# Optimization experiments

Measured on AMD Instinct MI355X. Metric: run time of the kernel, lower is better.

## Reference

```python
import jax, jax.numpy as jnp
import numpy as np

B, LQ, LK, DQ, DK, DV, H = 4, 256, 512, 256, 256, 256, 128


def setup_inputs() -> dict:
    key = jax.random.key(0)
    kq, kk, kv, kwq, kwk, kwv, kl = jax.random.split(key, 7)
    queries = jax.random.normal(kq, (B, LQ, DQ), dtype=jnp.float32)
    keys = jax.random.normal(kk, (B, LK, DK), dtype=jnp.float32)
    values = jax.random.normal(kv, (B, LK, DV), dtype=jnp.float32)
    # Lazy linear params (no bias): W_q: DQ->H, W_k: DK->H, w_v: H->1
    Wq = jax.random.normal(kwq, (DQ, H), dtype=jnp.float32) / np.sqrt(DQ)
    Wk = jax.random.normal(kwk, (DK, H), dtype=jnp.float32) / np.sqrt(DK)
    wv = jax.random.normal(kwv, (H,), dtype=jnp.float32) / np.sqrt(H)
    valid_lens = jax.random.randint(kl, (B,), 1, LK + 1)
    return {"queries": queries, "keys": keys, "values": values,
            "Wq": Wq, "Wk": Wk, "wv": wv, "valid_lens": valid_lens}


def reference(queries, keys, values, Wq, Wk, wv, valid_lens):
    q = jnp.einsum('bqd,dh->bqh', queries, Wq)          # [B,LQ,H]
    k = jnp.einsum('bkd,dh->bkh', keys, Wk)             # [B,LK,H]
    # broadcast-add -> tanh -> reduce over H (the big [B,LQ,LK,H] intermediate)
    features = jnp.tanh(q[:, :, None, :] + k[:, None, :, :])
    scores = jnp.einsum('bqkh,h->bqk', features, wv)    # [B,LQ,LK]
    # masked_softmax with per-batch valid lengths (d2l semantics: masked -> -1e6)
    mask = jnp.arange(scores.shape[-1])[None, None, :] < valid_lens[:, None, None]
    scores = jnp.where(mask, scores, jnp.float32(-1e6))
    attn = jax.nn.softmax(scores, axis=-1)              # [B,LQ,LK]
    return jnp.einsum('bqk,bkv->bqv', attn, values)     # [B,LQ,DV]
```

## Files before the change

### kernel.cpp

```cpp
#include <hip/hip_runtime.h>

#define B_   4
#define LQ_  256
#define LK_  512
#define DQK_ 256
#define DV_  256
#define H_   128

#define TANH_C 2.8853900817779268f
#define L2E    1.4426950408889634f
#define NQBLK (B_ * LQ_ / 4)
#define NKBLK (B_ * LK_ / 4)

__global__ __launch_bounds__(128) void proj_kernel(const float* __restrict__ Q,
                                                   const float* __restrict__ K,
                                                   const float* __restrict__ Wq,
                                                   const float* __restrict__ Wk,
                                                   float* __restrict__ eq,
                                                   float* __restrict__ ekT) {
    const int blk = blockIdx.x;
    const bool isq = blk < NQBLK;
    const float* in = isq ? Q  : K;
    const float* W  = isq ? Wq : Wk;
    const int r0 = (isq ? blk : blk - NQBLK) * 4;
    const int t  = threadIdx.x;

    float acc0 = 0.f, acc1 = 0.f, acc2 = 0.f, acc3 = 0.f;
    const float4* in4 = reinterpret_cast<const float4*>(in + (size_t)r0 * DQK_);
    for (int d4 = 0; d4 < DQK_ / 4; ++d4) {
        float4 r0v = in4[0 * (DQK_ / 4) + d4];
        float4 r1v = in4[1 * (DQK_ / 4) + d4];
        float4 r2v = in4[2 * (DQK_ / 4) + d4];
        float4 r3v = in4[3 * (DQK_ / 4) + d4];
#pragma unroll
        for (int e = 0; e < 4; ++e) {
            float w = W[(size_t)(4 * d4 + e) * H_ + t];
            acc0 = fmaf(reinterpret_cast<const float*>(&r0v)[e], w, acc0);
            acc1 = fmaf(reinterpret_cast<const float*>(&r1v)[e], w, acc1);
            acc2 = fmaf(reinterpret_cast<const float*>(&r2v)[e], w, acc2);
            acc3 = fmaf(reinterpret_cast<const float*>(&r3v)[e], w, acc3);
        }
    }
    float e0 = __builtin_amdgcn_exp2f(acc0 * TANH_C);
    float e1 = __builtin_amdgcn_exp2f(acc1 * TANH_C);
    float e2 = __builtin_amdgcn_exp2f(acc2 * TANH_C);
    float e3 = __builtin_amdgcn_exp2f(acc3 * TANH_C);
    if (isq) {
        eq[(size_t)(r0 + 0) * H_ + t] = e0;
        eq[(size_t)(r0 + 1) * H_ + t] = e1;
        eq[(size_t)(r0 + 2) * H_ + t] = e2;
        eq[(size_t)(r0 + 3) * H_ + t] = e3;
    } else {
        const int b  = r0 >> 9;
        const int k0 = r0 & (LK_ - 1);
        float* o = ekT + ((size_t)(b * H_ + t)) * LK_ + k0;
        *reinterpret_cast<float4*>(o) = make_float4(e0, e1, e2, e3);
    }
}

__global__ __launch_bounds__(1024) void attn_kernel(
    const float* __restrict__ eq,
    const float* __restrict__ ekT,
    const float* __restrict__ wv,
    const float* __restrict__ values,
    const int*   __restrict__ valid_lens,
    float* __restrict__ out) {
    __shared__ float eq_l[4][H_];
    __shared__ float wm2[H_];
    __shared__ float sc[LK_][4];
    __shared__ float part[4][4][DV_];
    __shared__ float red[20];
    __shared__ float inv_s[4];

    const int blk = blockIdx.x;
    const int b   = blk >> 6;
    const int qt  = blk & 63;
    const int t   = threadIdx.x;

    if (t < 512) {
        eq_l[t >> 7][t & 127] = eq[(size_t)(b * LQ_ + qt * 4 + (t >> 7)) * H_ + (t & 127)];
    } else if (t < 640) {
        wm2[t - 512] = -2.f * wv[t - 512];
    }
    __syncthreads();

    const int valid = valid_lens[b];

    {
        const int k    = t & 511;
        const int pair = __builtin_amdgcn_readfirstlane(t >> 9);
        float2 s2 = make_float2(-1e6f, -1e6f);
        if (k < valid) {
            const float* ekp = ekT + (size_t)b * H_ * LK_ + k;
            const float4* w4  = reinterpret_cast<const float4*>(wm2);
            const float4* qa4 = reinterpret_cast<const float4*>(eq_l[2 * pair]);
            const float4* qb4 = reinterpret_cast<const float4*>(eq_l[2 * pair + 1]);
            float p0 = 0.f, p1 = 0.f;
#pragma unroll 4
            for (int h4 = 0; h4 < H_ / 4; ++h4) {
                float4 w  = w4[h4];
                float4 qa = qa4[h4];
                float4 qb = qb4[h4];
#pragma unroll
                for (int e = 0; e < 4; ++e) {
                    float ek = ekp[(size_t)(4 * h4 + e) * LK_];
                    float fa = fmaf(reinterpret_cast<const float*>(&qa)[e], ek, 1.f);
                    float fb = fmaf(reinterpret_cast<const float*>(&qb)[e], ek, 1.f);
                    float ww = reinterpret_cast<const float*>(&w)[e];
                    p0 = fmaf(ww, __builtin_amdgcn_rcpf(fa), p0);
                    p1 = fmaf(ww, __builtin_amdgcn_rcpf(fb), p1);
                }
            }
            s2 = make_float2(p0, p1);
        }
        *reinterpret_cast<float2*>(&sc[k][2 * pair]) = s2;
    }
    __syncthreads();

    const int qi = t >> 8;
    const int kl = t & 255;
    float s0 = sc[kl][qi], s1 = sc[kl + 256][qi];
    {
        float m = fmaxf(s0, s1);
#pragma unroll
        for (int off = 32; off; off >>= 1) m = fmaxf(m, __shfl_down(m, off, 64));
        if ((t & 63) == 0) red[t >> 6] = m;
    }
    __syncthreads();
    if (t < 4) {
        red[16 + t] = fmaxf(fmaxf(red[4 * t], red[4 * t + 1]),
                            fmaxf(red[4 * t + 2], red[4 * t + 3]));
    }
    __syncthreads();
    {
        const float m = red[16 + qi];
        float e0 = __builtin_amdgcn_exp2f((s0 - m) * L2E);
        float e1 = __builtin_amdgcn_exp2f((s1 - m) * L2E);
        sc[kl][qi]       = e0;
        sc[kl + 256][qi] = e1;
        float ss = e0 + e1;
#pragma unroll
        for (int off = 32; off; off >>= 1) ss += __shfl_down(ss, off, 64);
        if ((t & 63) == 0) red[t >> 6] = ss;
    }
    __syncthreads();
    if (t < 4) {
        inv_s[t] = 1.f / (red[4 * t] + red[4 * t + 1] + red[4 * t + 2] + red[4 * t + 3]);
    }
    __syncthreads();

    {
        const int kh = __builtin_amdgcn_readfirstlane(t >> 8);
        const int v  = t & 255;
        const int kstart = kh * 128;
        const int kend   = min(kstart + 128, valid);
        const float* vb = values + (size_t)b * LK_ * DV_ + v;
        float a0 = 0.f, a1 = 0.f, a2 = 0.f, a3 = 0.f;
#pragma unroll 4
        for (int k = kstart; k < kend; ++k) {
            float4 f  = *reinterpret_cast<const float4*>(&sc[k][0]);
            float val = vb[(size_t)k * DV_];
            a0 = fmaf(f.x, val, a0);
            a1 = fmaf(f.y, val, a1);
            a2 = fmaf(f.z, val, a2);
            a3 = fmaf(f.w, val, a3);
        }
        part[kh][0][v] = a0;
        part[kh][1][v] = a1;
        part[kh][2][v] = a2;
        part[kh][3][v] = a3;
    }
    __syncthreads();
    {
        const int v = t & 255;
        float r = (part[0][qi][v] + part[1][qi][v]) + (part[2][qi][v] + part[3][qi][v]);
        out[(size_t)(b * LQ_ + qt * 4 + qi) * DV_ + v] = r * inv_s[qi];
    }
}

extern "C" void kernel_launch(void* const* d_in, const int* in_sizes, int n_in,
                              void* d_out, int out_size, void* d_ws, size_t ws_size,
                              hipStream_t stream) {
    const float* queries    = (const float*)d_in[0];
    const float* keys       = (const float*)d_in[1];
    const float* values     = (const float*)d_in[2];
    const float* Wq         = (const float*)d_in[3];
    const float* Wk         = (const float*)d_in[4];
    const float* wv         = (const float*)d_in[5];
    const int*   valid_lens = (const int*)d_in[6];
    float* out = (float*)d_out;

    float* eq  = (float*)d_ws;
    float* ekT = eq + (size_t)B_ * LQ_ * H_;

    proj_kernel<<<NQBLK + NKBLK, 128, 0, stream>>>(queries, keys, Wq, Wk, eq, ekT);
    attn_kernel<<<B_ * LQ_ / 4, 1024, 0, stream>>>(eq, ekT, wv, values, valid_lens, out);
}
```

Before: 30.44 us.

## Retile projection to 8 rows via LDS and attention to 2 queries per block

The projection kernel now stages 8 input rows in shared memory and computes 8 outputs per thread, halving the block count and reusing each weight load across more rows. The attention kernel is retiled to 512-thread blocks handling 2 queries each, with every thread scoring 2 adjacent keys via float2 loads. The block index is swizzled so adjacent blocks interleave batches. The eq/wv staging in LDS is dropped in favour of direct uniform loads. The aim is better occupancy and more blocks, at the cost of each block re-reading ekT and values for only 2 queries, which doubles global traffic for those tensors.

Measured after the change: 41.54 us. 36.4% more time.

```diff
diff --git a/kernel.cpp b/kernel.cpp
--- a/kernel.cpp
+++ b/kernel.cpp
@@ -9,8 +9,8 @@
 
 #define TANH_C 2.8853900817779268f
 #define L2E    1.4426950408889634f
-#define NQBLK (B_ * LQ_ / 4)
-#define NKBLK (B_ * LK_ / 4)
+#define NQBLK (B_ * LQ_ / 8)
+#define NKBLK (B_ * LK_ / 8)
 
 __global__ __launch_bounds__(128) void proj_kernel(const float* __restrict__ Q,
                                                    const float* __restrict__ K,
@@ -18,108 +18,94 @@
                                                    const float* __restrict__ Wk,
                                                    float* __restrict__ eq,
                                                    float* __restrict__ ekT) {
+    __shared__ float rows[8 * DQK_];
     const int blk = blockIdx.x;
     const bool isq = blk < NQBLK;
     const float* in = isq ? Q  : K;
     const float* W  = isq ? Wq : Wk;
-    const int r0 = (isq ? blk : blk - NQBLK) * 4;
+    const int r0 = (isq ? blk : blk - NQBLK) * 8;
     const int t  = threadIdx.x;
 
-    float acc0 = 0.f, acc1 = 0.f, acc2 = 0.f, acc3 = 0.f;
     const float4* in4 = reinterpret_cast<const float4*>(in + (size_t)r0 * DQK_);
+    float4* r4 = reinterpret_cast<float4*>(rows);
+#pragma unroll
+    for (int i = 0; i < 4; ++i) r4[t + 128 * i] = in4[t + 128 * i];
+    __syncthreads();
+
+    float acc[8];
+#pragma unroll
+    for (int j = 0; j < 8; ++j) acc[j] = 0.f;
+
+#pragma unroll 2
     for (int d4 = 0; d4 < DQK_ / 4; ++d4) {
-        float4 r0v = in4[0 * (DQK_ / 4) + d4];
-        float4 r1v = in4[1 * (DQK_ / 4) + d4];
-        float4 r2v = in4[2 * (DQK_ / 4) + d4];
-        float4 r3v = in4[3 * (DQK_ / 4) + d4];
+        float w0 = W[(size_t)(4 * d4 + 0) * H_ + t];
+        float w1 = W[(size_t)(4 * d4 + 1) * H_ + t];
+        float w2 = W[(size_t)(4 * d4 + 2) * H_ + t];
+        float w3 = W[(size_t)(4 * d4 + 3) * H_ + t];
 #pragma unroll
-        for (int e = 0; e < 4; ++e) {
-            float w = W[(size_t)(4 * d4 + e) * H_ + t];
-            acc0 = fmaf(reinterpret_cast<const float*>(&r0v)[e], w, acc0);
-            acc1 = fmaf(reinterpret_cast<const float*>(&r1v)[e], w, acc1);
-            acc2 = fmaf(reinterpret_cast<const float*>(&r2v)[e], w, acc2);
-            acc3 = fmaf(reinterpret_cast<const float*>(&r3v)[e], w, acc3);
+        for (int j = 0; j < 8; ++j) {
+            float4 r = *reinterpret_cast<const float4*>(&rows[j * DQK_ + 4 * d4]);
+            acc[j] = fmaf(r.x, w0, fmaf(r.y, w1, fmaf(r.z, w2, fmaf(r.w, w3, acc[j]))));
         }
     }
-    float e0 = __builtin_amdgcn_exp2f(acc0 * TANH_C);
-    float e1 = __builtin_amdgcn_exp2f(acc1 * TANH_C);
-    float e2 = __builtin_amdgcn_exp2f(acc2 * TANH_C);
-    float e3 = __builtin_amdgcn_exp2f(acc3 * TANH_C);
+    float e[8];
+#pragma unroll
+    for (int j = 0; j < 8; ++j) e[j] = __builtin_amdgcn_exp2f(acc[j] * TANH_C);
+
     if (isq) {
-        eq[(size_t)(r0 + 0) * H_ + t] = e0;
-        eq[(size_t)(r0 + 1) * H_ + t] = e1;
-        eq[(size_t)(r0 + 2) * H_ + t] = e2;
-        eq[(size_t)(r0 + 3) * H_ + t] = e3;
+#pragma unroll
+        for (int j = 0; j < 8; ++j)
+            eq[(size_t)(r0 + j) * H_ + t] = e[j];
     } else {
         const int b  = r0 >> 9;
         const int k0 = r0 & (LK_ - 1);
         float* o = ekT + ((size_t)(b * H_ + t)) * LK_ + k0;
-        *reinterpret_cast<float4*>(o) = make_float4(e0, e1, e2, e3);
+        *reinterpret_cast<float4*>(o)     = make_float4(e[0], e[1], e[2], e[3]);
+        *reinterpret_cast<float4*>(o + 4) = make_float4(e[4], e[5], e[6], e[7]);
     }
 }
 
-__global__ __launch_bounds__(1024) void attn_kernel(
+__global__ __launch_bounds__(512, 4) void attn_kernel(
     const float* __restrict__ eq,
     const float* __restrict__ ekT,
     const float* __restrict__ wv,
     const float* __restrict__ values,
     const int*   __restrict__ valid_lens,
     float* __restrict__ out) {
-    __shared__ float eq_l[4][H_];
-    __shared__ float wm2[H_];
-    __shared__ float sc[LK_][4];
-    __shared__ float part[4][4][DV_];
-    __shared__ float red[20];
-    __shared__ float inv_s[4];
+    __shared__ float sc[LK_][2];
+    __shared__ float part[2][2][DV_];
+    __shared__ float red[8];
+    __shared__ float redm[2];
+    __shared__ float inv_s[2];
 
     const int blk = blockIdx.x;
-    const int b   = blk >> 6;
-    const int qt  = blk & 63;
+    const int b   = (blk & 1) | (((blk >> 8) & 1) << 1);
+    const int qt  = (blk >> 1) & 127;
     const int t   = threadIdx.x;
-
-    if (t < 512) {
-        eq_l[t >> 7][t & 127] = eq[(size_t)(b * LQ_ + qt * 4 + (t >> 7)) * H_ + (t & 127)];
-    } else if (t < 640) {
-        wm2[t - 512] = -2.f * wv[t - 512];
-    }
-    __syncthreads();
-
     const int valid = valid_lens[b];
 
+    const int qi = __builtin_amdgcn_readfirstlane(t >> 8);
+    const int kq = t & 255;
+
+    float s0 = -1e6f, s1 = -1e6f;
     {
-        const int k    = t & 511;
-        const int pair = __builtin_amdgcn_readfirstlane(t >> 9);
-        float2 s2 = make_float2(-1e6f, -1e6f);
-        if (k < valid) {
-            const float* ekp = ekT + (size_t)b * H_ * LK_ + k;
-            const float4* w4  = reinterpret_cast<const float4*>(wm2);
-            const float4* qa4 = reinterpret_cast<const float4*>(eq_l[2 * pair]);
-            const float4* qb4 = reinterpret_cast<const float4*>(eq_l[2 * pair + 1]);
+        const float* eqr = eq + (size_t)(b * LQ_ + qt * 2 + qi) * H_;
+        const float* ekp = ekT + (size_t)b * H_ * LK_ + 2 * kq;
+        if (2 * kq < valid) {
             float p0 = 0.f, p1 = 0.f;
-#pragma unroll 4
-            for (int h4 = 0; h4 < H_ / 4; ++h4) {
-                float4 w  = w4[h4];
-                float4 qa = qa4[h4];
-                float4 qb = qb4[h4];
-#pragma unroll
-                for (int e = 0; e < 4; ++e) {
-                    float ek = ekp[(size_t)(4 * h4 + e) * LK_];
-                    float fa = fmaf(reinterpret_cast<const float*>(&qa)[e], ek, 1.f);
-                    float fb = fmaf(reinterpret_cast<const float*>(&qb)[e], ek, 1.f);
-                    float ww = reinterpret_cast<const float*>(&w)[e];
-                    p0 = fmaf(ww, __builtin_amdgcn_rcpf(fa), p0);
-                    p1 = fmaf(ww, __builtin_amdgcn_rcpf(fb), p1);
-                }
+#pragma unroll 8
+            for (int h = 0; h < H_; ++h) {
+                float2 ek = *reinterpret_cast<const float2*>(ekp + (size_t)h * LK_);
+                float q = eqr[h];
+                float w = wv[h];
+                p0 = fmaf(w, __builtin_amdgcn_rcpf(fmaf(q, ek.x, 1.f)), p0);
+                p1 = fmaf(w, __builtin_amdgcn_rcpf(fmaf(q, ek.y, 1.f)), p1);
             }
-            s2 = make_float2(p0, p1);
+            s0 = -2.f * p0;
+            s1 = (2 * kq + 1 < valid) ? -2.f * p1 : -1e6f;
         }
-        *reinterpret_cast<float2*>(&sc[k][2 * pair]) = s2;
     }
-    __syncthreads();
 
-    const int qi = t >> 8;
-    const int kl = t & 255;
-    float s0 = sc[kl][qi], s1 = sc[kl + 256][qi];
     {
         float m = fmaxf(s0, s1);
 #pragma unroll
@@ -127,54 +113,48 @@
         if ((t & 63) == 0) red[t >> 6] = m;
     }
     __syncthreads();
-    if (t < 4) {
-        red[16 + t] = fmaxf(fmaxf(red[4 * t], red[4 * t + 1]),
-                            fmaxf(red[4 * t + 2], red[4 * t + 3]));
+    if (t < 2) {
+        redm[t] = fmaxf(fmaxf(red[4 * t], red[4 * t + 1]),
+                        fmaxf(red[4 * t + 2], red[4 * t + 3]));
     }
     __syncthreads();
     {
-        const float m = red[16 + qi];
+        const float m = redm[qi];
         float e0 = __builtin_amdgcn_exp2f((s0 - m) * L2E);
         float e1 = __builtin_amdgcn_exp2f((s1 - m) * L2E);
-        sc[kl][qi]       = e0;
-        sc[kl + 256][qi] = e1;
+        sc[2 * kq][qi]     = e0;
+        sc[2 * kq + 1][qi] = e1;
         float ss = e0 + e1;
 #pragma unroll
         for (int off = 32; off; off >>= 1) ss += __shfl_down(ss, off, 64);
         if ((t & 63) == 0) red[t >> 6] = ss;
     }
     __syncthreads();
-    if (t < 4) {
+    if (t < 2) {
         inv_s[t] = 1.f / (red[4 * t] + red[4 * t + 1] + red[4 * t + 2] + red[4 * t + 3]);
     }
     __syncthreads();
 
     {
-        const int kh = __builtin_amdgcn_readfirstlane(t >> 8);
-        const int v  = t & 255;
-        const int kstart = kh * 128;
-        const int kend   = min(kstart + 128, valid);
+        const int v    = t & 255;
+        const int half = t >> 8;
         const float* vb = values + (size_t)b * LK_ * DV_ + v;
-        float a0 = 0.f, a1 = 0.f, a2 = 0.f, a3 = 0.f;
-#pragma unroll 4
-        for (int k = kstart; k < kend; ++k) {
-            float4 f  = *reinterpret_cast<const float4*>(&sc[k][0]);
+        float a0 = 0.f, a1 = 0.f;
+#pragma unroll 8
+        for (int k = half; k < valid; k += 2) {
+            float2 w  = *reinterpret_cast<const float2*>(&sc[k][0]);
             float val = vb[(size_t)k * DV_];
-            a0 = fmaf(f.x, val, a0);
-            a1 = fmaf(f.y, val, a1);
-            a2 = fmaf(f.z, val, a2);
-            a3 = fmaf(f.w, val, a3);
+            a0 = fmaf(w.x, val, a0);
+            a1 = fmaf(w.y, val, a1);
         }
-        part[kh][0][v] = a0;
-        part[kh][1][v] = a1;
-        part[kh][2][v] = a2;
-        part[kh][3][v] = a3;
+        part[half][0][v] = a0;
+        part[half][1][v] = a1;
     }
     __syncthreads();
     {
         const int v = t & 255;
-        float r = (part[0][qi][v] + part[1][qi][v]) + (part[2][qi][v] + part[3][qi][v]);
-        out[(size_t)(b * LQ_ + qt * 4 + qi) * DV_ + v] = r * inv_s[qi];
+        out[(size_t)(b * LQ_ + qt * 2 + qi) * DV_ + v] =
+            (part[0][qi][v] + part[1][qi][v]) * inv_s[qi];
     }
 }
 
@@ -194,5 +174,5 @@
     float* ekT = eq + (size_t)B_ * LQ_ * H_;
 
     proj_kernel<<<NQBLK + NKBLK, 128, 0, stream>>>(queries, keys, Wq, Wk, eq, ekT);
-    attn_kernel<<<B_ * LQ_ / 4, 1024, 0, stream>>>(eq, ekT, wv, values, valid_lens, out);
+    attn_kernel<<<2 * B_ * LQ_ / 4, 512, 0, stream>>>(eq, ekT, wv, values, valid_lens, out);
 }
```

## Split attention into batch-balanced score kernel and separate PV kernel

Applied to the files above, without the earlier changes.

Splits the fused attention kernel into a score/softmax kernel and a separate attention-times-values kernel, with normalized weights passed through workspace memory. Each score block now handles one query position across all four batches, so work from short and long valid lengths lands in the same block. Inside that block, keys past the valid length skip the second half of the tanh loop. The cost is an extra kernel launch plus a global write and read of the attention matrix.

Measured after the change: 41.20 us. 1.35x slower.

```diff
diff --git a/kernel.cpp b/kernel.cpp
--- a/kernel.cpp
+++ b/kernel.cpp
@@ -58,94 +58,129 @@
     }
 }
 
-__global__ __launch_bounds__(1024) void attn_kernel(
+__global__ __launch_bounds__(1024) void score_kernel(
     const float* __restrict__ eq,
     const float* __restrict__ ekT,
     const float* __restrict__ wv,
+    const int*   __restrict__ valid_lens,
+    float* __restrict__ attw) {
+    __shared__ float eq_l[4][H_];
+    __shared__ float wm2[H_];
+    __shared__ float red[16];
+    __shared__ float redm[4];
+    __shared__ float inv_s[4];
+
+    const int qt = blockIdx.x;
+    const int t  = threadIdx.x;
+
+    if (t < 512) {
+        eq_l[t >> 7][t & 127] = eq[((size_t)(t >> 7) * LQ_ + qt) * H_ + (t & 127)];
+    } else if (t < 640) {
+        wm2[t - 512] = -2.f * wv[t - 512];
+    }
+    __syncthreads();
+
+    const int bb = __builtin_amdgcn_readfirstlane(t >> 8);
+    const int kq = t & 255;
+    const int valid = valid_lens[bb];
+
+    float s0 = -1e6f, s1 = -1e6f;
+    {
+        const float4* w4 = reinterpret_cast<const float4*>(wm2);
+        const float4* q4 = reinterpret_cast<const float4*>(eq_l[bb]);
+        const float* ekp = ekT + (size_t)bb * H_ * LK_ + kq;
+        if (kq < valid) {
+            if (kq + 256 < valid) {
+                float p0 = 0.f, p1 = 0.f;
+#pragma unroll 2
+                for (int h4 = 0; h4 < H_ / 4; ++h4) {
+                    float4 w = w4[h4];
+                    float4 q = q4[h4];
+#pragma unroll
+                    for (int e = 0; e < 4; ++e) {
+                        const float* base = ekp + (size_t)(4 * h4 + e) * LK_;
+                        float ek0 = base[0];
+                        float ek1 = base[256];
+                        float qq = reinterpret_cast<const float*>(&q)[e];
+                        float ww = reinterpret_cast<const float*>(&w)[e];
+                        p0 = fmaf(ww, __builtin_amdgcn_rcpf(fmaf(qq, ek0, 1.f)), p0);
+                        p1 = fmaf(ww, __builtin_amdgcn_rcpf(fmaf(qq, ek1, 1.f)), p1);
+                    }
+                }
+                s0 = p0; s1 = p1;
+            } else {
+                float p0 = 0.f;
+#pragma unroll 2
+                for (int h4 = 0; h4 < H_ / 4; ++h4) {
+                    float4 w = w4[h4];
+                    float4 q = q4[h4];
+#pragma unroll
+                    for (int e = 0; e < 4; ++e) {
+                        float ek0 = ekp[(size_t)(4 * h4 + e) * LK_];
+                        float qq = reinterpret_cast<const float*>(&q)[e];
+                        float ww = reinterpret_cast<const float*>(&w)[e];
+                        p0 = fmaf(ww, __builtin_amdgcn_rcpf(fmaf(qq, ek0, 1.f)), p0);
+                    }
+                }
+                s0 = p0;
+            }
+        }
+    }
+
+    const int w = t >> 6;
+    {
+        float m = fmaxf(s0, s1);
+#pragma unroll
+        for (int off = 32; off; off >>= 1) m = fmaxf(m, __shfl_down(m, off, 64));
+        if ((t & 63) == 0) red[w] = m;
+    }
+    __syncthreads();
+    if (t < 4) {
+        redm[t] = fmaxf(fmaxf(red[4 * t], red[4 * t + 1]),
+                        fmaxf(red[4 * t + 2], red[4 * t + 3]));
+    }
+    __syncthreads();
+    const float m = redm[bb];
+    float e0 = __builtin_amdgcn_exp2f((s0 - m) * L2E);
+    float e1 = __builtin_amdgcn_exp2f((s1 - m) * L2E);
+    {
+        float ss = e0 + e1;
+#pragma unroll
+        for (int off = 32; off; off >>= 1) ss += __shfl_down(ss, off, 64);
+        if ((t & 63) == 0) red[w] = ss;
+    }
+    __syncthreads();
+    if (t < 4) {
+        inv_s[t] = 1.f / (red[4 * t] + red[4 * t + 1] + red[4 * t + 2] + red[4 * t + 3]);
+    }
+    __syncthreads();
+    {
+        const float inv = inv_s[bb];
+        float* ap = attw + ((size_t)(bb * LQ_ + qt)) * LK_ + kq;
+        ap[0]   = e0 * inv;
+        ap[256] = e1 * inv;
+    }
+}
+
+__global__ __launch_bounds__(1024) void pv_kernel(
+    const float* __restrict__ attw,
     const float* __restrict__ values,
     const int*   __restrict__ valid_lens,
     float* __restrict__ out) {
-    __shared__ float eq_l[4][H_];
-    __shared__ float wm2[H_];
     __shared__ float sc[LK_][4];
     __shared__ float part[4][4][DV_];
-    __shared__ float red[20];
-    __shared__ float inv_s[4];
 
     const int blk = blockIdx.x;
     const int b   = blk >> 6;
     const int qt  = blk & 63;
     const int t   = threadIdx.x;
-
-    if (t < 512) {
-        eq_l[t >> 7][t & 127] = eq[(size_t)(b * LQ_ + qt * 4 + (t >> 7)) * H_ + (t & 127)];
-    } else if (t < 640) {
-        wm2[t - 512] = -2.f * wv[t - 512];
-    }
-    __syncthreads();
-
     const int valid = valid_lens[b];
 
-    {
-        const int k    = t & 511;
-        const int pair = __builtin_amdgcn_readfirstlane(t >> 9);
-        float2 s2 = make_float2(-1e6f, -1e6f);
-        if (k < valid) {
-            const float* ekp = ekT + (size_t)b * H_ * LK_ + k;
-            const float4* w4  = reinterpret_cast<const float4*>(wm2);
-            const float4* qa4 = reinterpret_cast<const float4*>(eq_l[2 * pair]);
-            const float4* qb4 = reinterpret_cast<const float4*>(eq_l[2 * pair + 1]);
-            float p0 = 0.f, p1 = 0.f;
-#pragma unroll 4
-            for (int h4 = 0; h4 < H_ / 4; ++h4) {
-                float4 w  = w4[h4];
-                float4 qa = qa4[h4];
-                float4 qb = qb4[h4];
-#pragma unroll
-                for (int e = 0; e < 4; ++e) {
-                    float ek = ekp[(size_t)(4 * h4 + e) * LK_];
-                    float fa = fmaf(reinterpret_cast<const float*>(&qa)[e], ek, 1.f);
-                    float fb = fmaf(reinterpret_cast<const float*>(&qb)[e], ek, 1.f);
-                    float ww = reinterpret_cast<const float*>(&w)[e];
-                    p0 = fmaf(ww, __builtin_amdgcn_rcpf(fa), p0);
-                    p1 = fmaf(ww, __builtin_amdgcn_rcpf(fb), p1);
-                }
-            }
-            s2 = make_float2(p0, p1);
-        }
-        *reinterpret_cast<float2*>(&sc[k][2 * pair]) = s2;
-    }
-    __syncthreads();
-
-    const int qi = t >> 8;
-    const int kl = t & 255;
-    float s0 = sc[kl][qi], s1 = sc[kl + 256][qi];
-    {
-        float m = fmaxf(s0, s1);
-#pragma unroll
-        for (int off = 32; off; off >>= 1) m = fmaxf(m, __shfl_down(m, off, 64));
-        if ((t & 63) == 0) red[t >> 6] = m;
-    }
-    __syncthreads();
-    if (t < 4) {
-        red[16 + t] = fmaxf(fmaxf(red[4 * t], red[4 * t + 1]),
-                            fmaxf(red[4 * t + 2], red[4 * t + 3]));
-    }
-    __syncthreads();
-    {
-        const float m = red[16 + qi];
-        float e0 = __builtin_amdgcn_exp2f((s0 - m) * L2E);
-        float e1 = __builtin_amdgcn_exp2f((s1 - m) * L2E);
-        sc[kl][qi]       = e0;
-        sc[kl + 256][qi] = e1;
-        float ss = e0 + e1;
-#pragma unroll
-        for (int off = 32; off; off >>= 1) ss += __shfl_down(ss, off, 64);
-        if ((t & 63) == 0) red[t >> 6] = ss;
-    }
-    __syncthreads();
-    if (t < 4) {
-        inv_s[t] = 1.f / (red[4 * t] + red[4 * t + 1] + red[4 * t + 2] + red[4 * t + 3]);
+#pragma unroll
+    for (int i = 0; i < 2; ++i) {
+        int idx = t + 1024 * i;
+        int r = idx >> 9, k = idx & 511;
+        sc[k][r] = attw[((size_t)(b * LQ_ + qt * 4 + r)) * LK_ + k];
     }
     __syncthreads();
 
@@ -172,9 +207,10 @@
     }
     __syncthreads();
     {
-        const int v = t & 255;
-        float r = (part[0][qi][v] + part[1][qi][v]) + (part[2][qi][v] + part[3][qi][v]);
-        out[(size_t)(b * LQ_ + qt * 4 + qi) * DV_ + v] = r * inv_s[qi];
+        const int qi = t >> 8;
+        const int v  = t & 255;
+        out[(size_t)(b * LQ_ + qt * 4 + qi) * DV_ + v] =
+            (part[0][qi][v] + part[1][qi][v]) + (part[2][qi][v] + part[3][qi][v]);
     }
 }
 
@@ -190,9 +226,11 @@
     const int*   valid_lens = (const int*)d_in[6];
     float* out = (float*)d_out;
 
-    float* eq  = (float*)d_ws;
-    float* ekT = eq + (size_t)B_ * LQ_ * H_;
-
-    proj_kernel<<<NQBLK + NKBLK, 128, 0, stream>>>(queries, keys, Wq, Wk, eq, ekT);
-    attn_kernel<<<B_ * LQ_ / 4, 1024, 0, stream>>>(eq, ekT, wv, values, valid_lens, out);
-}
+    float* eq   = (float*)d_ws;
+    float* ekT  = eq  + (size_t)B_ * LQ_ * H_;
+    float* attw = ekT + (size_t)B_ * H_ * LK_;
+
+    proj_kernel <<<NQBLK + NKBLK, 128, 0, stream>>>(queries, keys, Wq, Wk, eq, ekT);
+    score_kernel<<<LQ_, 1024, 0, stream>>>(eq, ekT, wv, valid_lens, attw);
+    pv_kernel   <<<B_ * LQ_ / 4, 1024, 0, stream>>>(attw, values, valid_lens, out);
+}
```
